# Kernel tuning notes

Hardware: AMD Instinct MI355X
Metric: run time of the kernel (lower is better)

Reference implementation:

```python
import jax, jax.numpy as jnp
import numpy as np

D = 384
H = 6
DK = D // H
EPS = 1e-5


def _layernorm(x, g, b):
    mu = jnp.mean(x, axis=-1, keepdims=True)
    var = jnp.var(x, axis=-1, keepdims=True)
    return (x - mu) * jax.lax.rsqrt(var + EPS) * g + b


def setup_inputs() -> dict:
    key = jax.random.key(0)
    ks = jax.random.split(key, 12)
    B, N = 8, 2048
    s = lambda fan_in: 1.0 / np.sqrt(fan_in)
    return {
        "points": jax.random.normal(ks[0], (B, 3 + D, N), dtype=jnp.float32),
        "ln1_g": jnp.ones((D,), jnp.float32),
        "ln1_b": jnp.zeros((D,), jnp.float32),
        "w_qkv": jax.random.uniform(ks[1], (3 * D, D), jnp.float32, -s(D), s(D)),
        "w_o": jax.random.uniform(ks[2], (D, D), jnp.float32, -s(D), s(D)),
        "b_o": jnp.zeros((D,), jnp.float32),
        "ln2_g": jnp.ones((D,), jnp.float32),
        "ln2_b": jnp.zeros((D,), jnp.float32),
        "w1": jax.random.uniform(ks[3], (2 * D, D), jnp.float32, -s(D), s(D)),
        "b1": jnp.zeros((2 * D,), jnp.float32),
        "w2": jax.random.uniform(ks[4], (D, 2 * D), jnp.float32, -s(2 * D), s(2 * D)),
        "b2": jnp.zeros((D,), jnp.float32),
    }


def reference(points, ln1_g, ln1_b, w_qkv, w_o, b_o, ln2_g, ln2_b, w1, b1, w2, b2):
    coords = points[:, :3, :]                       # [B, 3, N]
    feats = jnp.transpose(points[:, 3:, :], (0, 2, 1))  # [B, N, D]
    B, N, _ = feats.shape

    # pre-norm + fused QKV projection (no bias)
    h = _layernorm(feats, ln1_g, ln1_b)
    qkv = jnp.einsum('bnd,ed->bne', h, w_qkv)       # [B, N, 3D]
    q, k, v = jnp.split(qkv, 3, axis=-1)

    split_heads = lambda t: jnp.transpose(t.reshape(B, N, H, DK), (0, 2, 1, 3))
    q, k, v = split_heads(q), split_heads(k), split_heads(v)  # [B, H, N, DK]

    scale = DK ** -0.5
    scores = jnp.einsum('bhid,bhjd->bhij', q, k) * scale      # [B, H, N, N]
    attn = jax.nn.softmax(scores, axis=-1)
    ctx = jnp.einsum('bhij,bhjd->bhid', attn, v)              # [B, H, N, DK]
    ctx = jnp.transpose(ctx, (0, 2, 1, 3)).reshape(B, N, D)
    attn_out = jnp.einsum('bnd,ed->bne', ctx, w_o) + b_o

    x = feats + attn_out
    # FFN with exact (erf) GELU, hidden = 2*D
    h2 = _layernorm(x, ln2_g, ln2_b)
    ff = jnp.einsum('bnd,ed->bne', h2, w1) + b1
    ff = jax.nn.gelu(ff, approximate=False)
    ff = jnp.einsum('bne,de->bnd', ff, w2) + b2
    x = x + ff

    return jnp.concatenate([coords, jnp.transpose(x, (0, 2, 1))], axis=1)
```

## Files before the change

### kernel.cpp

```cpp
#include <hip/hip_runtime.h>
#include <cstdint>


typedef __bf16 bf16;
typedef __bf16 bf16x8 __attribute__((ext_vector_type(8)));
typedef __bf16 bf16x4 __attribute__((ext_vector_type(4)));
typedef short s16x4 __attribute__((ext_vector_type(4)));
typedef float floatx4 __attribute__((ext_vector_type(4)));
typedef uint32_t __attribute__((address_space(1))) gu32;
typedef uint32_t __attribute__((address_space(3))) lu32;

#define NN 2048
#define DD 384
#define HH 6
#define DK 64
#define BB 8
#define MM (BB * NN)
#define D3 (3 * DD)
#define D2 (2 * DD)
#define CH (3 + DD)
#define LP 72
#define LPV 136

#define QSCALE 0.18033688011112042f

static __device__ __forceinline__ s16x4 as_s16x4(bf16x4 v) {
    union { bf16x4 b; s16x4 s; } u; u.b = v; return u.s;
}


__global__ void cast_all_kernel(const float* __restrict__ w_qkv, const float* __restrict__ w_o,
                                const float* __restrict__ w1, const float* __restrict__ w2,
                                bf16* __restrict__ o_qkv, bf16* __restrict__ o_o,
                                bf16* __restrict__ o_w1, bf16* __restrict__ o_w2) {
    int i = blockIdx.x * 256 + threadIdx.x;
    if (i < 442368) o_qkv[i] = (bf16)w_qkv[i];
    else if (i < 589824) o_o[i - 442368] = (bf16)w_o[i - 442368];
    else if (i < 884736) o_w1[i - 589824] = (bf16)w1[i - 589824];
    else o_w2[i - 884736] = (bf16)w2[i - 884736];
}

__global__ void coords_kernel(const float* __restrict__ pts, float* __restrict__ out) {
    int i = blockIdx.x * 256 + threadIdx.x;
    int b = i / (3 * NN), r = i % (3 * NN);
    out[(size_t)b * CH * NN + r] = pts[(size_t)b * CH * NN + r];
}

__global__ void transpose_kernel(const float* __restrict__ pts, float* __restrict__ feats) {
    __shared__ float T[32][33];
    int n0 = blockIdx.x * 32, d0 = blockIdx.y * 32, b = blockIdx.z;
    int tx = threadIdx.x, ty = threadIdx.y;
    const float* src = pts + (size_t)b * CH * NN;
#pragma unroll
    for (int i = 0; i < 4; ++i)
        T[ty + i * 8][tx] = src[(size_t)(3 + d0 + ty + i * 8) * NN + n0 + tx];
    __syncthreads();
    float* dst = feats + (size_t)b * NN * DD;
#pragma unroll
    for (int i = 0; i < 4; ++i)
        dst[(size_t)(n0 + ty + i * 8) * DD + d0 + tx] = T[tx][ty + i * 8];
}

__global__ __launch_bounds__(256) void ln_kernel(const float* __restrict__ x,
                                                 const float* __restrict__ g,
                                                 const float* __restrict__ bta,
                                                 bf16* __restrict__ out) {
    int wave = threadIdx.x >> 6, lane = threadIdx.x & 63;
    int row = blockIdx.x * 4 + wave;
    const float* xr = x + (size_t)row * DD;
    float v[6], s = 0.f, sq = 0.f;
#pragma unroll
    for (int i = 0; i < 6; ++i) { v[i] = xr[lane + i * 64]; s += v[i]; sq += v[i] * v[i]; }
#pragma unroll
    for (int o = 1; o < 64; o <<= 1) { s += __shfl_xor(s, o); sq += __shfl_xor(sq, o); }
    float mu = s * (1.f / DD);
    float var = sq * (1.f / DD) - mu * mu;
    float rs = rsqrtf(var + 1e-5f);
    bf16* orow = out + (size_t)row * DD;
#pragma unroll
    for (int i = 0; i < 6; ++i) {
        int d = lane + i * 64;
        orow[d] = (bf16)((v[i] - mu) * rs * g[d] + bta[d]);
    }
}

template <int NC, int K, int MODE, int TN>
__global__ __launch_bounds__(256, 2)
void gemm_bt(const bf16* __restrict__ A, const bf16* __restrict__ W,
             const float* __restrict__ bias, const float* __restrict__ res,
             bf16* __restrict__ obf, float* __restrict__ of32, bf16* __restrict__ vt) {
    constexpr int MI = (TN == 128) ? 4 : 2;
    __shared__ bf16 As[128 * 32];
    __shared__ bf16 Ws[TN * 32];
    const int t = threadIdx.x;
    const int wave = t >> 6, lane = t & 63;
    const int m0 = blockIdx.x * 128, n0 = blockIdx.y * TN;
    const int wm = (TN == 128) ? (wave >> 1) * 64 : wave * 32;
    const int wn = (TN == 128) ? (wave & 1) * 64 : 0;
    const int lr = lane & 15, quad = lane >> 4;
    const int sr = t >> 2, sc = (t & 3) * 8;

    floatx4 acc[MI][4];
#pragma unroll
    for (int mi = 0; mi < MI; ++mi)
#pragma unroll
        for (int ni = 0; ni < 4; ++ni) {
            floatx4 z = {0.f, 0.f, 0.f, 0.f};
            acc[mi][ni] = z;
        }

    for (int k0 = 0; k0 < K; k0 += 32) {
        __syncthreads();
#pragma unroll
        for (int i = 0; i < 2; ++i) {
            const int r = i * 64 + sr;
            __builtin_amdgcn_global_load_lds(
                (const gu32*)&A[(size_t)(m0 + r) * K + k0 + sc],
                (lu32*)&As[r * 32 + sc], 16, 0, 0);
        }
#pragma unroll
        for (int i = 0; i < TN / 64; ++i) {
            const int r = i * 64 + sr;
            __builtin_amdgcn_global_load_lds(
                (const gu32*)&W[(size_t)(n0 + r) * K + k0 + sc],
                (lu32*)&Ws[r * 32 + sc], 16, 0, 0);
        }
        __syncthreads();
        bf16x8 af[MI], bfr[4];
#pragma unroll
        for (int mi = 0; mi < MI; ++mi)
            af[mi] = *(const bf16x8*)&As[(wm + mi * 16 + lr) * 32 + quad * 8];
#pragma unroll
        for (int ni = 0; ni < 4; ++ni)
            bfr[ni] = *(const bf16x8*)&Ws[(wn + ni * 16 + lr) * 32 + quad * 8];
#pragma unroll
        for (int mi = 0; mi < MI; ++mi)
#pragma unroll
            for (int ni = 0; ni < 4; ++ni)
                acc[mi][ni] = __builtin_amdgcn_mfma_f32_16x16x32_bf16(af[mi], bfr[ni], acc[mi][ni], 0, 0, 0);
    }

#pragma unroll
    for (int mi = 0; mi < MI; ++mi) {
#pragma unroll
        for (int ni = 0; ni < 4; ++ni) {
            const int r0 = m0 + wm + mi * 16 + quad * 4;
            const int c = n0 + wn + ni * 16 + lr;
            floatx4 v = acc[mi][ni];
            if constexpr (MODE == 0) {
                const int cb = n0 + wn + ni * 16;
                if (cb >= 2 * DD) {
                    const int hh = (c - 2 * DD) >> 6, dk = (c - 2 * DD) & 63;
                    const int b = r0 >> 11, n = r0 & (NN - 1);
                    bf16x4 pk;
#pragma unroll
                    for (int r = 0; r < 4; ++r) pk[r] = (bf16)v[r];
                    *(bf16x4*)&vt[((size_t)(b * HH + hh) * DK + dk) * NN + n] = pk;
                } else {
                    const float sc_q = (cb < DD) ? QSCALE : 1.0f;
#pragma unroll
                    for (int r = 0; r < 4; ++r) obf[(size_t)(r0 + r) * NC + c] = (bf16)(v[r] * sc_q);
                }
            } else if constexpr (MODE == 1) {
#pragma unroll
                for (int r = 0; r < 4; ++r)
                    of32[(size_t)(r0 + r) * NC + c] = v[r] + bias[c] + res[(size_t)(r0 + r) * NC + c];
            } else if constexpr (MODE == 2) {
#pragma unroll
                for (int r = 0; r < 4; ++r) {
                    float u = v[r] + bias[c];
                    obf[(size_t)(r0 + r) * NC + c] = (bf16)(0.5f * u * (1.f + erff(u * 0.70710678118f)));
                }
            } else {
                const int b = r0 >> 11, n = r0 & (NN - 1);
                float o4[4];
#pragma unroll
                for (int r = 0; r < 4; ++r)
                    o4[r] = v[r] + bias[c] + res[(size_t)(r0 + r) * DD + c];
                float4 val = make_float4(o4[0], o4[1], o4[2], o4[3]);
                *(float4*)&of32[((size_t)b * CH + 3 + c) * NN + n] = val;
            }
        }
    }
}

__global__ __launch_bounds__(256, 3)
void attn_kernel(const bf16* __restrict__ qkv, const bf16* __restrict__ vt,
                 bf16* __restrict__ ctx) {
    __shared__ bf16 Ks[128 * LP];
    __shared__ bf16 Vs[64 * LPV];
    const int t = threadIdx.x, wave = t >> 6, lane = t & 63;
    const int lr = lane & 15, quad = lane >> 4;
    const int bh = blockIdx.y, b = bh / HH, h = bh % HH;
    const int q0 = blockIdx.x * 128 + wave * 32;
    const bf16* qbase = qkv + (size_t)b * NN * D3 + h * DK;
    const bf16* kbase = qbase + DD;
    const bf16* vbase = vt + (size_t)bh * DK * NN;

    bf16x8 aq[2][2];
#pragma unroll
    for (int mi = 0; mi < 2; ++mi)
#pragma unroll
        for (int ks = 0; ks < 2; ++ks)
            aq[mi][ks] = *(const bf16x8*)&qbase[(size_t)(q0 + mi * 16 + lr) * D3 +
                                                ks * 32 + quad * 8];

    bf16x4 ones4;
#pragma unroll
    for (int i = 0; i < 4; ++i) ones4[i] = (bf16)1.0f;
    const s16x4 ones_s = as_s16x4(ones4);

    floatx4 o[2][4], ol[2];
#pragma unroll
    for (int mi = 0; mi < 2; ++mi) {
        floatx4 z = {0.f, 0.f, 0.f, 0.f};
        ol[mi] = z;
#pragma unroll
        for (int nd = 0; nd < 4; ++nd) o[mi][nd] = z;
    }

    for (int j0 = 0; j0 < NN; j0 += 128) {
        __syncthreads();
        {
            const int rr = t >> 3, cc = (t & 7) * 8;
#pragma unroll
            for (int i = 0; i < 4; ++i) {
                const int j = i * 32 + rr;
                *(bf16x8*)&Ks[j * LP + cc] =
                    *(const bf16x8*)&kbase[(size_t)(j0 + j) * D3 + cc];
            }
            const int rr2 = t >> 4, cc2 = (t & 15) * 8;
#pragma unroll
            for (int i = 0; i < 4; ++i) {
                const int d = i * 16 + rr2;
                *(bf16x8*)&Vs[d * LPV + cc2] =
                    *(const bf16x8*)&vbase[(size_t)d * NN + j0 + cc2];
            }
        }
        __syncthreads();

        floatx4 s[2][8];
#pragma unroll
        for (int mi = 0; mi < 2; ++mi)
#pragma unroll
            for (int nj = 0; nj < 8; ++nj) {
                floatx4 z = {0.f, 0.f, 0.f, 0.f};
                s[mi][nj] = z;
            }
#pragma unroll
        for (int ks = 0; ks < 2; ++ks)
#pragma unroll
            for (int nj = 0; nj < 8; ++nj) {
                bf16x8 bk = *(const bf16x8*)&Ks[(nj * 16 + lr) * LP + ks * 32 + quad * 8];
#pragma unroll
                for (int mi = 0; mi < 2; ++mi)
                    s[mi][nj] = __builtin_amdgcn_mfma_f32_16x16x32_bf16(bk, aq[mi][ks],
                                                                        s[mi][nj], 0, 0, 0);
            }

#pragma unroll
        for (int nj = 0; nj < 8; ++nj) {
            s16x4 ap[2];
#pragma unroll
            for (int mi = 0; mi < 2; ++mi) {
                bf16x4 pk;
#pragma unroll
                for (int r = 0; r < 4; ++r) pk[r] = (bf16)exp2f(s[mi][nj][r]);
                ap[mi] = as_s16x4(pk);
            }
#pragma unroll
            for (int nd = 0; nd < 4; ++nd) {
                s16x4 bv = as_s16x4(*(const bf16x4*)&Vs[(nd * 16 + lr) * LPV +
                                                        nj * 16 + quad * 4]);
#pragma unroll
                for (int mi = 0; mi < 2; ++mi)
                    o[mi][nd] = __builtin_amdgcn_mfma_f32_16x16x16bf16_1k(ap[mi], bv,
                                                                          o[mi][nd], 0, 0, 0);
            }
#pragma unroll
            for (int mi = 0; mi < 2; ++mi)
                ol[mi] = __builtin_amdgcn_mfma_f32_16x16x16bf16_1k(ap[mi], ones_s, ol[mi], 0, 0, 0);
        }
    }

#pragma unroll
    for (int mi = 0; mi < 2; ++mi)
#pragma unroll
        for (int r = 0; r < 4; ++r) {
            const int n = q0 + mi * 16 + quad * 4 + r;
            const float inv = 1.0f / ol[mi][r];
#pragma unroll
            for (int nd = 0; nd < 4; ++nd) {
                const int d = h * DK + nd * 16 + lr;
                ctx[(size_t)(b * NN + n) * DD + d] = (bf16)(o[mi][nd][r] * inv);
            }
        }
}


extern "C" void kernel_launch(void* const* d_in, const int* in_sizes, int n_in,
                              void* d_out, int out_size, void* d_ws, size_t ws_size,
                              hipStream_t stream) {
    const float* points = (const float*)d_in[0];
    const float* ln1_g = (const float*)d_in[1];
    const float* ln1_b = (const float*)d_in[2];
    const float* w_qkv = (const float*)d_in[3];
    const float* w_o   = (const float*)d_in[4];
    const float* b_o   = (const float*)d_in[5];
    const float* ln2_g = (const float*)d_in[6];
    const float* ln2_b = (const float*)d_in[7];
    const float* w1    = (const float*)d_in[8];
    const float* b1    = (const float*)d_in[9];
    const float* w2    = (const float*)d_in[10];
    const float* b2    = (const float*)d_in[11];
    float* out = (float*)d_out;

    char* ws = (char*)d_ws;
    size_t off = 0;
    auto alloc = [&](size_t bytes) -> void* {
        void* p = ws + off;
        off += (bytes + 255) & ~(size_t)255;
        return p;
    };
    float* feats = (float*)alloc((size_t)MM * DD * 4);
    float* xbuf  = (float*)alloc((size_t)MM * DD * 4);
    bf16* h1     = (bf16*)alloc((size_t)MM * DD * 2);
    bf16* h2     = (bf16*)alloc((size_t)MM * DD * 2);
    bf16* qkvb   = (bf16*)alloc((size_t)MM * D3 * 2);
    bf16* vtb    = (bf16*)alloc((size_t)BB * HH * DK * NN * 2);
    bf16* ctx    = (bf16*)alloc((size_t)MM * DD * 2);
    bf16* ffh    = (bf16*)alloc((size_t)MM * D2 * 2);
    bf16* wqkv_bf = (bf16*)alloc((size_t)D3 * DD * 2);
    bf16* wo_bf   = (bf16*)alloc((size_t)DD * DD * 2);
    bf16* w1_bf   = (bf16*)alloc((size_t)D2 * DD * 2);
    bf16* w2_bf   = (bf16*)alloc((size_t)DD * D2 * 2);

    cast_all_kernel<<<1179648 / 256, 256, 0, stream>>>(w_qkv, w_o, w1, w2,
                                                       wqkv_bf, wo_bf, w1_bf, w2_bf);
    coords_kernel<<<(BB * 3 * NN) / 256, 256, 0, stream>>>(points, out);
    transpose_kernel<<<dim3(NN / 32, DD / 32, BB), dim3(32, 8), 0, stream>>>(points, feats);
    ln_kernel<<<MM / 4, 256, 0, stream>>>(feats, ln1_g, ln1_b, h1);
    gemm_bt<D3, DD, 0, 128><<<dim3(MM / 128, D3 / 128), 256, 0, stream>>>(
        h1, wqkv_bf, nullptr, nullptr, qkvb, nullptr, vtb);
    attn_kernel<<<dim3(NN / 128, BB * HH), 256, 0, stream>>>(qkvb, vtb, ctx);
    gemm_bt<DD, DD, 1, 64><<<dim3(MM / 128, DD / 64), 256, 0, stream>>>(
        ctx, wo_bf, b_o, feats, nullptr, xbuf, nullptr);
    ln_kernel<<<MM / 4, 256, 0, stream>>>(xbuf, ln2_g, ln2_b, h2);
    gemm_bt<D2, DD, 2, 128><<<dim3(MM / 128, D2 / 128), 256, 0, stream>>>(
        h2, w1_bf, b1, nullptr, ffh, nullptr, nullptr);
    gemm_bt<DD, D2, 3, 64><<<dim3(MM / 128, DD / 64), 256, 0, stream>>>(
        ffh, w2_bf, b2, xbuf, nullptr, out, nullptr);
}
```

Measured before the change: 289.8 us.

## Store GEMM and attention tiles in MFMA fragment order via direct global-to-LDS loads

Shared-memory tiles in the GEMM and attention kernels move from padded row-major layouts to a per-16-row fragment layout, where each lane's 16-byte fragment sits contiguously at lane*8. The attention kernel's K and V tile loads switch from register-staged copies to global_load_lds direct-to-LDS transfers. LDS reads become conflict-free linear accesses, and the register round trip and its address arithmetic go away in attention. In exchange, each wave now issues global loads that touch 16 rows with 64-byte segments, so global coalescing may suffer.

```diff
diff --git a/kernel.cpp b/kernel.cpp
--- a/kernel.cpp
+++ b/kernel.cpp
@@ -19,8 +19,6 @@
 #define D3 (3 * DD)
 #define D2 (2 * DD)
 #define CH (3 + DD)
-#define LP 72
-#define LPV 136
 
 #define QSCALE 0.18033688011112042f
 
@@ -90,15 +88,17 @@
              const float* __restrict__ bias, const float* __restrict__ res,
              bf16* __restrict__ obf, float* __restrict__ of32, bf16* __restrict__ vt) {
     constexpr int MI = (TN == 128) ? 4 : 2;
-    __shared__ bf16 As[128 * 32];
-    __shared__ bf16 Ws[TN * 32];
+    constexpr int NBW = TN / 16;
+    __shared__ bf16 As[8 * 512];
+    __shared__ bf16 Ws[NBW * 512];
     const int t = threadIdx.x;
     const int wave = t >> 6, lane = t & 63;
     const int m0 = blockIdx.x * 128, n0 = blockIdx.y * TN;
     const int wm = (TN == 128) ? (wave >> 1) * 64 : wave * 32;
     const int wn = (TN == 128) ? (wave & 1) * 64 : 0;
+    const int abase = wm >> 4;
+    const int bbase = wn >> 4;
     const int lr = lane & 15, quad = lane >> 4;
-    const int sr = t >> 2, sc = (t & 3) * 8;
 
     floatx4 acc[MI][4];
 #pragma unroll
@@ -113,26 +113,26 @@
         __syncthreads();
 #pragma unroll
         for (int i = 0; i < 2; ++i) {
-            const int r = i * 64 + sr;
+            const int blk = i * 4 + wave;
             __builtin_amdgcn_global_load_lds(
-                (const gu32*)&A[(size_t)(m0 + r) * K + k0 + sc],
-                (lu32*)&As[r * 32 + sc], 16, 0, 0);
-        }
-#pragma unroll
-        for (int i = 0; i < TN / 64; ++i) {
-            const int r = i * 64 + sr;
+                (const gu32*)&A[(size_t)(m0 + blk * 16 + lr) * K + k0 + quad * 8],
+                (lu32*)&As[blk * 512], 16, 0, 0);
+        }
+#pragma unroll
+        for (int i = 0; i < NBW / 4; ++i) {
+            const int blk = i * 4 + wave;
             __builtin_amdgcn_global_load_lds(
-                (const gu32*)&W[(size_t)(n0 + r) * K + k0 + sc],
-                (lu32*)&Ws[r * 32 + sc], 16, 0, 0);
+                (const gu32*)&W[(size_t)(n0 + blk * 16 + lr) * K + k0 + quad * 8],
+                (lu32*)&Ws[blk * 512], 16, 0, 0);
         }
         __syncthreads();
         bf16x8 af[MI], bfr[4];
 #pragma unroll
         for (int mi = 0; mi < MI; ++mi)
-            af[mi] = *(const bf16x8*)&As[(wm + mi * 16 + lr) * 32 + quad * 8];
+            af[mi] = *(const bf16x8*)&As[(abase + mi) * 512 + lane * 8];
 #pragma unroll
         for (int ni = 0; ni < 4; ++ni)
-            bfr[ni] = *(const bf16x8*)&Ws[(wn + ni * 16 + lr) * 32 + quad * 8];
+            bfr[ni] = *(const bf16x8*)&Ws[(bbase + ni) * 512 + lane * 8];
 #pragma unroll
         for (int mi = 0; mi < MI; ++mi)
 #pragma unroll
@@ -187,8 +187,8 @@
 __global__ __launch_bounds__(256, 3)
 void attn_kernel(const bf16* __restrict__ qkv, const bf16* __restrict__ vt,
                  bf16* __restrict__ ctx) {
-    __shared__ bf16 Ks[128 * LP];
-    __shared__ bf16 Vs[64 * LPV];
+    __shared__ bf16 Ksf[16 * 512];
+    __shared__ bf16 Vsf[16 * 512];
     const int t = threadIdx.x, wave = t >> 6, lane = t & 63;
     const int lr = lane & 15, quad = lane >> 4;
     const int bh = blockIdx.y, b = bh / HH, h = bh % HH;
@@ -221,21 +221,21 @@
 
     for (int j0 = 0; j0 < NN; j0 += 128) {
         __syncthreads();
-        {
-            const int rr = t >> 3, cc = (t & 7) * 8;
-#pragma unroll
-            for (int i = 0; i < 4; ++i) {
-                const int j = i * 32 + rr;
-                *(bf16x8*)&Ks[j * LP + cc] =
-                    *(const bf16x8*)&kbase[(size_t)(j0 + j) * D3 + cc];
-            }
-            const int rr2 = t >> 4, cc2 = (t & 15) * 8;
-#pragma unroll
-            for (int i = 0; i < 4; ++i) {
-                const int d = i * 16 + rr2;
-                *(bf16x8*)&Vs[d * LPV + cc2] =
-                    *(const bf16x8*)&vbase[(size_t)d * NN + j0 + cc2];
-            }
+#pragma unroll
+        for (int i = 0; i < 4; ++i) {
+            const int idx = i * 4 + wave;
+            __builtin_amdgcn_global_load_lds(
+                (const gu32*)&kbase[(size_t)(j0 + (idx >> 1) * 16 + lr) * D3 +
+                                    (idx & 1) * 32 + quad * 8],
+                (lu32*)&Ksf[idx * 512], 16, 0, 0);
+        }
+#pragma unroll
+        for (int i = 0; i < 4; ++i) {
+            const int idx = i * 4 + wave;
+            __builtin_amdgcn_global_load_lds(
+                (const gu32*)&vbase[(size_t)((idx >> 2) * 16 + lr) * NN +
+                                    j0 + (idx & 3) * 32 + quad * 8],
+                (lu32*)&Vsf[idx * 512], 16, 0, 0);
         }
         __syncthreads();
 
@@ -251,7 +251,7 @@
         for (int ks = 0; ks < 2; ++ks)
 #pragma unroll
             for (int nj = 0; nj < 8; ++nj) {
-                bf16x8 bk = *(const bf16x8*)&Ks[(nj * 16 + lr) * LP + ks * 32 + quad * 8];
+                bf16x8 bk = *(const bf16x8*)&Ksf[(nj * 2 + ks) * 512 + lane * 8];
 #pragma unroll
                 for (int mi = 0; mi < 2; ++mi)
                     s[mi][nj] = __builtin_amdgcn_mfma_f32_16x16x32_bf16(bk, aq[mi][ks],
@@ -270,8 +270,9 @@
             }
 #pragma unroll
             for (int nd = 0; nd < 4; ++nd) {
-                s16x4 bv = as_s16x4(*(const bf16x4*)&Vs[(nd * 16 + lr) * LPV +
-                                                        nj * 16 + quad * 4]);
+                s16x4 bv = as_s16x4(*(const bf16x4*)&Vsf[
+                    (nd * 4 + (nj >> 1)) * 512 + ((nj & 1) * 2 + (quad >> 1)) * 128 +
+                    lr * 8 + (quad & 1) * 4]);
 #pragma unroll
                 for (int mi = 0; mi < 2; ++mi)
                     o[mi][nd] = __builtin_amdgcn_mfma_f32_16x16x16bf16_1k(ap[mi], bv,
```

Measured after the change: 326.4 us. 12.6% more time.
